# Kernel optimization log

Hardware: AMD Instinct MI355X
Metric: run time of the kernel (lower is better)

## Reference

```python
import jax, jax.numpy as jnp
import numpy as np

FEATURES = 1024
NUM_HEADS = 16
HEAD_SIZE = FEATURES // NUM_HEADS
B, T = 4, 2048
LN_EPS = 1e-6


def setup_inputs() -> dict:
    key = jax.random.key(0)
    ks = jax.random.split(key, 12)
    C, H, D = FEATURES, NUM_HEADS, HEAD_SIZE
    s_in = 1.0 / np.sqrt(C)
    s_ff = 1.0 / np.sqrt(4 * C)
    return {
        "x": jax.random.normal(ks[0], (B, T, C), jnp.float32),
        # per-head Q/K/V projections (no bias), stacked over heads
        "wq": jax.random.normal(ks[1], (H, C, D), jnp.float32) * s_in,
        "wk": jax.random.normal(ks[2], (H, C, D), jnp.float32) * s_in,
        "wv": jax.random.normal(ks[3], (H, C, D), jnp.float32) * s_in,
        "w_proj": jax.random.normal(ks[4], (C, C), jnp.float32) * s_in,
        "b_proj": jnp.zeros((C,), jnp.float32),
        "w_ff1": jax.random.normal(ks[5], (C, 4 * C), jnp.float32) * s_in,
        "b_ff1": jnp.zeros((4 * C,), jnp.float32),
        "w_ff2": jax.random.normal(ks[6], (4 * C, C), jnp.float32) * s_ff,
        "b_ff2": jnp.zeros((C,), jnp.float32),
        "ln1_scale": jnp.ones((C,), jnp.float32),
        "ln1_bias": jnp.zeros((C,), jnp.float32),
        "ln2_scale": jnp.ones((C,), jnp.float32),
        "ln2_bias": jnp.zeros((C,), jnp.float32),
    }


def _layernorm(x, scale, bias):
    mu = jnp.mean(x, axis=-1, keepdims=True)
    var = jnp.mean(jnp.square(x - mu), axis=-1, keepdims=True)
    return (x - mu) * jax.lax.rsqrt(var + LN_EPS) * scale + bias


def reference(x, wq, wk, wv, w_proj, b_proj, w_ff1, b_ff1, w_ff2, b_ff2,
              ln1_scale, ln1_bias, ln2_scale, ln2_bias):
    Bn, Tn, C = x.shape
    res = x
    xn = _layernorm(x, ln1_scale, ln1_bias)
    # per-head projections, vectorized over heads: [B,H,T,D]
    q = jnp.einsum('btc,hcd->bhtd', xn, wq)
    k = jnp.einsum('btc,hcd->bhtd', xn, wk)
    v = jnp.einsum('btc,hcd->bhtd', xn, wv)
    wei = jnp.einsum('bhtd,bhsd->bhts', q, k)
    tril = jnp.tril(jnp.ones((Tn, Tn), jnp.float32))
    # NOTE: original scales by C**-0.5 (full feature dim, not head_size),
    # and multiplies after masking (-inf * scale stays -inf).
    wei = jnp.where(tril == 0, -jnp.inf, wei) * (C ** -0.5)
    wei = jax.nn.softmax(wei, axis=-1)
    out = jnp.einsum('bhts,bhsd->bhtd', wei, v)
    # concat heads back to [B,T,C]
    out = out.transpose(0, 2, 1, 3).reshape(Bn, Tn, C)
    x = res + out @ w_proj + b_proj
    res = x
    xn = _layernorm(x, ln2_scale, ln2_bias)
    h = jax.nn.relu(xn @ w_ff1 + b_ff1)
    out = res + h @ w_ff2 + b_ff2
    return out
```

## Files before the change

kernel.cpp:

```cpp
#include <hip/hip_runtime.h>

#define Bn 4
#define Tn 2048
#define Cn 1024
#define Hn 16
#define Dn 64
#define Mr (Bn*Tn)

typedef _Float16 half8 __attribute__((ext_vector_type(8)));
typedef _Float16 half4v __attribute__((ext_vector_type(4)));
typedef float f32x4 __attribute__((ext_vector_type(4)));
typedef unsigned u32x4 __attribute__((ext_vector_type(4)));

__device__ __forceinline__ void g2l16(const void* g, void* l) {
  __builtin_amdgcn_global_load_lds((__attribute__((address_space(1))) void*)g,
                                   (__attribute__((address_space(3))) void*)l, 16, 0, 0);
}

#define SB  __builtin_amdgcn_sched_barrier(0)
#define BAR __builtin_amdgcn_s_barrier()
#define VMW8 asm volatile("s_waitcnt vmcnt(8)" ::: "memory")
#define VMW6 asm volatile("s_waitcnt vmcnt(6)" ::: "memory")
#define VMW4 asm volatile("s_waitcnt vmcnt(4)" ::: "memory")
#define VMW3 asm volatile("s_waitcnt vmcnt(3)" ::: "memory")
#define VMW0 asm volatile("s_waitcnt vmcnt(0)" ::: "memory")

__global__ __launch_bounds__(256) void transpose_f32_f16(const float* __restrict__ in,
                                                         _Float16* __restrict__ out,
                                                         int R, int C) {
  __shared__ float tile[32][33];
  const size_t zoff = (size_t)blockIdx.z * R * C;
  in += zoff; out += zoff;
  const int c0 = blockIdx.x * 32, r0 = blockIdx.y * 32;
  const int tx = threadIdx.x, ty = threadIdx.y;
#pragma unroll
  for (int i = 0; i < 4; ++i)
    tile[ty + i*8][tx] = in[(size_t)(r0 + ty + i*8) * C + c0 + tx];
  __syncthreads();
#pragma unroll
  for (int i = 0; i < 4; ++i)
    out[(size_t)(c0 + ty + i*8) * R + r0 + tx] = (_Float16)tile[tx][ty + i*8];
}

__global__ __launch_bounds__(256) void ln_row(const float* __restrict__ x,
                                              const float* __restrict__ g,
                                              const float* __restrict__ bta,
                                              _Float16* __restrict__ out) {
  const int row = blockIdx.x;
  const float4 v = ((const float4*)(x + (size_t)row * Cn))[threadIdx.x];
  float s  = v.x + v.y + v.z + v.w;
  float ss = v.x*v.x + v.y*v.y + v.z*v.z + v.w*v.w;
#pragma unroll
  for (int m = 1; m < 64; m <<= 1) { s += __shfl_xor(s, m); ss += __shfl_xor(ss, m); }
  __shared__ float red[8];
  const int wave = threadIdx.x >> 6, lane = threadIdx.x & 63;
  if (lane == 0) { red[wave] = s; red[4 + wave] = ss; }
  __syncthreads();
  s  = red[0] + red[1] + red[2] + red[3];
  ss = red[4] + red[5] + red[6] + red[7];
  const float mean = s * (1.0f/Cn);
  const float var  = ss * (1.0f/Cn) - mean*mean;
  const float rstd = rsqrtf(var + 1e-6f);
  const int c = threadIdx.x * 4;
  const float4 gg = ((const float4*)g)[threadIdx.x];
  const float4 bb = ((const float4*)bta)[threadIdx.x];
  half4v o;
  o[0] = (_Float16)((v.x - mean) * rstd * gg.x + bb.x);
  o[1] = (_Float16)((v.y - mean) * rstd * gg.y + bb.y);
  o[2] = (_Float16)((v.z - mean) * rstd * gg.z + bb.z);
  o[3] = (_Float16)((v.w - mean) * rstd * gg.w + bb.w);
  *((half4v*)(out + (size_t)row * Cn + c)) = o;
}

enum { EPI_QKV = 0, EPI_PROJ = 2, EPI_FF1 = 3, EPI_FF2 = 4 };

template<int BN, int EPI>
__global__ __launch_bounds__(512, 2) void gemm8p(const _Float16* __restrict__ A,
                                                 const _Float16* __restrict__ Bt,
                                                 void* __restrict__ outp,
                                                 void* __restrict__ out2,
                                                 void* __restrict__ out3,
                                                 const float* __restrict__ bias,
                                                 const float* __restrict__ resid,
                                                 int M, int N, int K, int nxg) {
  constexpr int NF = BN/64;
  constexpr int BSLOT = BN*32;
  __shared__ __align__(16) _Float16 Ar[4*256*32];
  __shared__ __align__(16) _Float16 Br[4*BSLOT];

  const int tid = threadIdx.x, wave = tid >> 6, lane = tid & 63;
  const int lr = lane & 15, lg = lane >> 4;
  const int sL = (lr & 3) ^ ((lr >> 2) & 3);
  const int laneoff = lr*32 + ((lg ^ sL) * 8);

  int lin = blockIdx.x;
  const int cpx = gridDim.x >> 3;
  lin = (lin & 7) * cpx + (lin >> 3);
  const int bx = lin % nxg, by = lin / nxg;
  const int brow = by * 256, bcol = bx * BN;
  const int wr = wave >> 2, wc = wave & 3;
  const int arow0 = wr * 128;
  const int bcol0 = wc * (BN/4);

  f32x4 acc[8][NF] = {};

  auto STAGE = [&](int st, int kh) {
    const int slot = (2*st + kh) & 3;
    const int koff = st*64 + kh*32;
#pragma unroll
    for (int i = 0; i < 2; ++i) {
      const int qc = i*512 + wave*64 + lane;
      const int row = qc >> 2;
      const int c = (qc & 3) ^ ((row & 3) ^ ((row >> 2) & 3));
      g2l16(A + (size_t)(brow + row)*K + koff + c*8,
            &Ar[slot*8192 + (i*512 + wave*64)*8]);
    }
#pragma unroll
    for (int i = 0; i < BN/128; ++i) {
      const int qc = i*512 + wave*64 + lane;
      const int row = qc >> 2;
      const int c = (qc & 3) ^ ((row & 3) ^ ((row >> 2) & 3));
      g2l16(Bt + (size_t)(bcol + row)*K + koff + c*8,
            &Br[slot*BSLOT + (i*512 + wave*64)*8]);
    }
  };
  auto RDA = [&](int slot, int mh, half8* af) {
#pragma unroll
    for (int i = 0; i < 4; ++i)
      af[i] = *(const half8*)(&Ar[slot*8192 + (arow0 + (mh*4 + i)*16)*32 + laneoff]);
  };
  auto RDB = [&](int slot, half8* bf) {
#pragma unroll
    for (int j = 0; j < NF; ++j)
      bf[j] = *(const half8*)(&Br[slot*BSLOT + (bcol0 + j*16)*32 + laneoff]);
  };

#define MMC(MH) do {                                                          \
    __builtin_amdgcn_s_setprio(1);                                            \
    _Pragma("unroll") for (int i_ = 0; i_ < 4; ++i_)                          \
      _Pragma("unroll") for (int j_ = 0; j_ < NF; ++j_)                       \
        acc[(MH)*4 + i_][j_] = __builtin_amdgcn_mfma_f32_16x16x32_f16(        \
            af[i_], bf[j_], acc[(MH)*4 + i_][j_], 0, 0, 0);                   \
    __builtin_amdgcn_s_setprio(0); } while (0)

  const int ns = K >> 6;
  STAGE(0, 0); STAGE(0, 1); STAGE(1, 0);
  if constexpr (BN == 256) VMW8; else VMW6;
  SB; BAR;

  half8 af[4], bf[NF];
  for (int s = 0; s < ns - 2; ++s) {
    const int s0 = (2*s) & 3, s1 = s0 + 1;
    RDB(s0, bf); RDA(s0, 0, af); STAGE(s + 1, 1);
    SB; BAR; MMC(0); SB; BAR;
    RDA(s0, 1, af);
    if constexpr (BN == 256) VMW8; else VMW6;
    SB; BAR; MMC(1); SB; BAR;
    RDB(s1, bf); RDA(s1, 0, af); STAGE(s + 2, 0);
    SB; BAR; MMC(0); SB; BAR;
    RDA(s1, 1, af);
    if constexpr (BN == 256) VMW8; else VMW6;
    SB; BAR; MMC(1); SB; BAR;
  }
  {
    const int s = ns - 2; const int s0 = (2*s) & 3, s1 = s0 + 1;
    RDB(s0, bf); RDA(s0, 0, af); STAGE(s + 1, 1);
    SB; BAR; MMC(0); SB; BAR;
    RDA(s0, 1, af);
    if constexpr (BN == 256) VMW8; else VMW6;
    SB; BAR; MMC(1); SB; BAR;
    RDB(s1, bf); RDA(s1, 0, af);
    SB; BAR; MMC(0); SB; BAR;
    RDA(s1, 1, af);
    if constexpr (BN == 256) VMW4; else VMW3;
    SB; BAR; MMC(1); SB; BAR;
  }
  {
    const int s = ns - 1; const int s0 = (2*s) & 3, s1 = s0 + 1;
    RDB(s0, bf); RDA(s0, 0, af);
    SB; BAR; MMC(0); SB; BAR;
    RDA(s0, 1, af);
    VMW0;
    SB; BAR; MMC(1); SB; BAR;
    RDB(s1, bf); RDA(s1, 0, af);
    SB; BAR; MMC(0); SB; BAR;
    RDA(s1, 1, af);
    SB; BAR; MMC(1); SB; BAR;
  }
#undef MMC

#pragma unroll
  for (int a = 0; a < 8; ++a) {
#pragma unroll
    for (int j = 0; j < NF; ++j) {
      const int col = bcol + bcol0 + j*16 + lr;
#pragma unroll
      for (int r = 0; r < 4; ++r) {
        const int row = brow + arow0 + a*16 + lg*4 + r;
        const float v = acc[a][j][r];
        if constexpr (EPI == EPI_QKV) {
          const int sel = col >> 10;
          const int cw = col & 1023;
          const int hh = cw >> 6, dd = cw & 63;
          const size_t bhh = (size_t)(row >> 11) * Hn + hh;
          const int t = row & 2047;
          if (sel == 0)      ((_Float16*)outp)[(bhh*Tn + t)*Dn + dd] = (_Float16)v;
          else if (sel == 1) ((_Float16*)out2)[(bhh*Tn + t)*Dn + dd] = (_Float16)v;
          else               ((_Float16*)out3)[(bhh*Dn + dd)*Tn + t] = (_Float16)v;
        } else if constexpr (EPI == EPI_PROJ || EPI == EPI_FF2) {
          ((float*)outp)[(size_t)row * N + col] = v + bias[col] + resid[(size_t)row * N + col];
        } else if constexpr (EPI == EPI_FF1) {
          const float t = v + bias[col];
          ((_Float16*)outp)[(size_t)row * N + col] = (_Float16)(t > 0.f ? t : 0.f);
        }
      }
    }
  }
}

__global__ __launch_bounds__(256) void attn_kernel(const _Float16* __restrict__ q,
                                                   const _Float16* __restrict__ k,
                                                   const _Float16* __restrict__ vt,
                                                   _Float16* __restrict__ out) {
  const int pi = blockIdx.x;
  const int qtA = pi * 128;
  const int qtB = (15 - pi) * 128;
  const int h = blockIdx.y, b = blockIdx.z;
  const int tid = threadIdx.x, wave = tid >> 6, lane = tid & 63;
  const int lr = lane & 15, lg = lane >> 4;
  const size_t bh = (size_t)b * Hn + h;
  const _Float16* qg = q  + bh * (Tn * Dn);
  const _Float16* kg = k  + bh * (Tn * Dn);
  const _Float16* vg = vt + bh * (Dn * Tn);

  __shared__ __align__(16) _Float16 Ks[2][64*64];
  __shared__ __align__(16) _Float16 Vs[2][64*64];

  const _Float16 qsc = (_Float16)0.03125f;
  half8 qfA[2][2], qfB[2][2];
#pragma unroll
  for (int qi = 0; qi < 2; ++qi)
#pragma unroll
    for (int dh = 0; dh < 2; ++dh) {
      half8 a = *(const half8*)(qg + (size_t)(qtA + wave*32 + qi*16 + lr)*Dn + dh*32 + lg*8);
      half8 c = *(const half8*)(qg + (size_t)(qtB + wave*32 + qi*16 + lr)*Dn + dh*32 + lg*8);
#pragma unroll
      for (int j = 0; j < 8; ++j) { a[j] *= qsc; c[j] *= qsc; }
      qfA[qi][dh] = a; qfB[qi][dh] = c;
    }

  f32x4 oaccA[2][4] = {}, oaccB[2][4] = {};
  float mrowA[2] = {-__builtin_inff(), -__builtin_inff()};
  float mrowB[2] = {-__builtin_inff(), -__builtin_inff()};
  float lsumA[2] = {0.f, 0.f}, lsumB[2] = {0.f, 0.f};

  const int ntB = (qtB >> 6) + 2;

  auto STAGE = [&](int bufi, int t) {
    const int kvt = t * 64;
#pragma unroll
    for (int r = 0; r < 2; ++r) {
      const int g0 = r*256 + wave*64;
      const int g  = g0 + lane;
      const int rr = g >> 3;
      const int cs = (g & 7) ^ (rr & 7);
      g2l16(kg + (size_t)(kvt + rr)*Dn + cs*8, &Ks[bufi][g0*8]);
      g2l16(vg + (size_t)rr*Tn + kvt + cs*8,   &Vs[bufi][g0*8]);
    }
  };

  auto COMPUTE = [&](const half8 (&qf)[2][2], f32x4 (&oacc)[2][4],
                     float* mrow, float* lsum, int qb,
                     const _Float16* KS, const _Float16* VS, int kvt) {
    half8 kb[4][2];
#pragma unroll
    for (int f = 0; f < 4; ++f)
#pragma unroll
      for (int dh = 0; dh < 2; ++dh)
        kb[f][dh] = *(const half8*)(KS + (16*f + lr)*64 + (((4*dh + lg) ^ (lr & 7)) * 8));

#pragma unroll
    for (int qi = 0; qi < 2; ++qi) {
      f32x4 sv[4];
#pragma unroll
      for (int f = 0; f < 4; ++f) {
        f32x4 tacc = {0.f, 0.f, 0.f, 0.f};
        tacc = __builtin_amdgcn_mfma_f32_16x16x32_f16(kb[f][0], qf[qi][0], tacc, 0, 0, 0);
        tacc = __builtin_amdgcn_mfma_f32_16x16x32_f16(kb[f][1], qf[qi][1], tacc, 0, 0, 0);
        sv[f] = tacc;
      }
      const int qrow = qb + wave*32 + qi*16 + lr;
#pragma unroll
      for (int f = 0; f < 4; ++f)
#pragma unroll
        for (int r = 0; r < 4; ++r) {
          const int kvv = kvt + 16*f + 4*lg + r;
          sv[f][r] = (kvv > qrow) ? -__builtin_inff() : sv[f][r];
        }
      float tm = sv[0][0];
#pragma unroll
      for (int f = 0; f < 4; ++f)
#pragma unroll
        for (int r = 0; r < 4; ++r) tm = fmaxf(tm, sv[f][r]);
      tm = fmaxf(tm, __shfl_xor(tm, 16));
      tm = fmaxf(tm, __shfl_xor(tm, 32));
      const float mn = fmaxf(mrow[qi], tm);
      const float alpha = __expf(mrow[qi] - mn);
      mrow[qi] = mn;
      float ps = 0.f;
#pragma unroll
      for (int f = 0; f < 4; ++f)
#pragma unroll
        for (int r = 0; r < 4; ++r) {
          const float e = __expf(sv[f][r] - mn);
          ps += e;
          sv[f][r] = e;
        }
      ps += __shfl_xor(ps, 16);
      ps += __shfl_xor(ps, 32);
      lsum[qi] = lsum[qi] * alpha + ps;
      unsigned ph[4][2];
#pragma unroll
      for (int f = 0; f < 4; ++f)
#pragma unroll
        for (int m = 0; m < 2; ++m) {
          const unsigned lo = (unsigned)__builtin_bit_cast(unsigned short, (_Float16)sv[f][2*m]);
          const unsigned hi = (unsigned)__builtin_bit_cast(unsigned short, (_Float16)sv[f][2*m + 1]);
          ph[f][m] = lo | (hi << 16);
        }
      float ab[4];
#pragma unroll
      for (int r = 0; r < 4; ++r) ab[r] = __shfl(alpha, 4*lg + r);
#pragma unroll
      for (int df = 0; df < 4; ++df)
#pragma unroll
        for (int r = 0; r < 4; ++r) oacc[qi][df][r] *= ab[r];
      const int s0 = lr + 16*(2*(lg & 1));
      const int s1 = s0 + 16;
      half8 pa[2];
#pragma unroll
      for (int kh = 0; kh < 2; ++kh) {
        u32x4 w = {0u, 0u, 0u, 0u};
#pragma unroll
        for (int fi = 0; fi < 2; ++fi) {
          const unsigned a0 = __shfl(ph[2*kh + fi][0], s0);
          const unsigned a1 = __shfl(ph[2*kh + fi][1], s0);
          const unsigned a2 = __shfl(ph[2*kh + fi][0], s1);
          const unsigned a3 = __shfl(ph[2*kh + fi][1], s1);
          const bool sel = ((lg >> 1) == fi);
          w[0] = sel ? a0 : w[0];
          w[1] = sel ? a1 : w[1];
          w[2] = sel ? a2 : w[2];
          w[3] = sel ? a3 : w[3];
        }
        pa[kh] = __builtin_bit_cast(half8, w);
      }
#pragma unroll
      for (int df = 0; df < 4; ++df) {
        half8 vb0 = *(const half8*)(VS + (16*df + lr)*64 + (((0 + lg) ^ (lr & 7)) * 8));
        half8 vb1 = *(const half8*)(VS + (16*df + lr)*64 + (((4 + lg) ^ (lr & 7)) * 8));
        oacc[qi][df] = __builtin_amdgcn_mfma_f32_16x16x32_f16(pa[0], vb0, oacc[qi][df], 0, 0, 0);
        oacc[qi][df] = __builtin_amdgcn_mfma_f32_16x16x32_f16(pa[1], vb1, oacc[qi][df], 0, 0, 0);
      }
    }
  };

  STAGE(0, 0);
  __syncthreads();

  for (int t = 0; t < ntB; ++t) {
    const int kvt = t * 64;
    if (t + 1 < ntB) STAGE((t + 1) & 1, t + 1);
    const _Float16* KS = Ks[t & 1];
    const _Float16* VS = Vs[t & 1];
    if (kvt <= qtA + wave*32 + 31) COMPUTE(qfA, oaccA, mrowA, lsumA, qtA, KS, VS, kvt);
    if (kvt <= qtB + wave*32 + 31) COMPUTE(qfB, oaccB, mrowB, lsumB, qtB, KS, VS, kvt);
    __syncthreads();
  }

  auto EPI = [&](const f32x4 (&oacc)[2][4], const float* lsum, int qb) {
#pragma unroll
    for (int qi = 0; qi < 2; ++qi) {
      const float linv = 1.0f / lsum[qi];
      float lb[4];
#pragma unroll
      for (int r = 0; r < 4; ++r) lb[r] = __shfl(linv, 4*lg + r);
#pragma unroll
      for (int df = 0; df < 4; ++df)
#pragma unroll
        for (int r = 0; r < 4; ++r) {
          const int row = qb + wave*32 + qi*16 + 4*lg + r;
          const int col = h*Dn + df*16 + lr;
          out[((size_t)b*Tn + row)*Cn + col] = (_Float16)(oacc[qi][df][r] * lb[r]);
        }
    }
  };
  EPI(oaccA, lsumA, qtA);
  EPI(oaccB, lsumB, qtB);
}

extern "C" void kernel_launch(void* const* d_in, const int* in_sizes, int n_in,
                              void* d_out, int out_size, void* d_ws, size_t ws_size,
                              hipStream_t stream) {
  const float* x      = (const float*)d_in[0];
  const float* wq     = (const float*)d_in[1];
  const float* wk     = (const float*)d_in[2];
  const float* wv     = (const float*)d_in[3];
  const float* w_proj = (const float*)d_in[4];
  const float* b_proj = (const float*)d_in[5];
  const float* w_ff1  = (const float*)d_in[6];
  const float* b_ff1  = (const float*)d_in[7];
  const float* w_ff2  = (const float*)d_in[8];
  const float* b_ff2  = (const float*)d_in[9];
  const float* ln1s   = (const float*)d_in[10];
  const float* ln1b   = (const float*)d_in[11];
  const float* ln2s   = (const float*)d_in[12];
  const float* ln2b   = (const float*)d_in[13];
  float* outp = (float*)d_out;

  char* ws = (char*)d_ws;
  constexpr size_t MB = (size_t)1 << 20;
  _Float16* Wq_t  = (_Float16*)(ws + 0*MB);
  _Float16* Wk_t  = (_Float16*)(ws + 2*MB);
  _Float16* Wv_t  = (_Float16*)(ws + 4*MB);
  _Float16* Wp_t  = (_Float16*)(ws + 6*MB);
  _Float16* Wf1_t = (_Float16*)(ws + 8*MB);
  _Float16* Wf2_t = (_Float16*)(ws + 16*MB);
  _Float16* xn    = (_Float16*)(ws + 24*MB);
  _Float16* attn_o= (_Float16*)(ws + 24*MB);
  _Float16* qbuf  = (_Float16*)(ws + 40*MB);
  _Float16* kbuf  = (_Float16*)(ws + 56*MB);
  _Float16* vtbuf = (_Float16*)(ws + 72*MB);
  _Float16* hbuf  = (_Float16*)(ws + 40*MB);
  float*    x2    = (float*)   (ws + 104*MB);
  _Float16* xn2   = (_Float16*)(ws + 136*MB);

  dim3 tb(32, 8);
  transpose_f32_f16<<<dim3(2, 32, 16), tb, 0, stream>>>(wq, Wq_t, 1024, 64);
  transpose_f32_f16<<<dim3(2, 32, 16), tb, 0, stream>>>(wk, Wk_t, 1024, 64);
  transpose_f32_f16<<<dim3(2, 32, 16), tb, 0, stream>>>(wv, Wv_t, 1024, 64);
  transpose_f32_f16<<<dim3(32, 32, 1), tb, 0, stream>>>(w_proj, Wp_t, 1024, 1024);
  transpose_f32_f16<<<dim3(128, 32, 1), tb, 0, stream>>>(w_ff1, Wf1_t, 1024, 4096);
  transpose_f32_f16<<<dim3(32, 128, 1), tb, 0, stream>>>(w_ff2, Wf2_t, 4096, 1024);

  ln_row<<<Mr, 256, 0, stream>>>(x, ln1s, ln1b, xn);

  gemm8p<256, EPI_QKV><<<dim3(384), 512, 0, stream>>>(xn, Wq_t, qbuf, kbuf, vtbuf,
                                                      nullptr, nullptr, Mr, 3*Cn, Cn, 12);

  attn_kernel<<<dim3(8, Hn, Bn), 256, 0, stream>>>(qbuf, kbuf, vtbuf, attn_o);

  gemm8p<128, EPI_PROJ><<<dim3(256), 512, 0, stream>>>(attn_o, Wp_t, x2, nullptr, nullptr,
                                                       b_proj, x, Mr, Cn, Cn, 8);

  ln_row<<<Mr, 256, 0, stream>>>(x2, ln2s, ln2b, xn2);

  gemm8p<256, EPI_FF1><<<dim3(512), 512, 0, stream>>>(xn2, Wf1_t, hbuf, nullptr, nullptr,
                                                      b_ff1, nullptr, Mr, 4*Cn, Cn, 16);
  gemm8p<128, EPI_FF2><<<dim3(256), 512, 0, stream>>>(hbuf, Wf2_t, outp, nullptr, nullptr,
                                                      b_ff2, x2, Mr, Cn, 4*Cn, 8);
}
```

Before: 592.7 us.

## Use exp2 softmax with lazy rescaling, skip masks off-diagonal, retile QKV GEMM

Folds log2(e) into the Q scale so softmax uses exp2f, and skips causal masking for tiles fully below the diagonal. It also rescales the output accumulators only when the running max grows beyond a threshold (lazy rescale), and packs probabilities with cvt_pkrtz. Separately it halves the QKV GEMM tile width to launch twice as many blocks. Lazy rescaling lets exponentials exceed 1 (up to about 2^11.5), which risks fp16 overflow or precision loss in P.

```diff
diff --git a/kernel.cpp b/kernel.cpp
--- a/kernel.cpp
+++ b/kernel.cpp
@@ -9,6 +9,7 @@
 
 typedef _Float16 half8 __attribute__((ext_vector_type(8)));
 typedef _Float16 half4v __attribute__((ext_vector_type(4)));
+typedef _Float16 half2v __attribute__((ext_vector_type(2)));
 typedef float f32x4 __attribute__((ext_vector_type(4)));
 typedef unsigned u32x4 __attribute__((ext_vector_type(4)));
 
@@ -236,7 +237,7 @@
   __shared__ __align__(16) _Float16 Ks[2][64*64];
   __shared__ __align__(16) _Float16 Vs[2][64*64];
 
-  const _Float16 qsc = (_Float16)0.03125f;
+  const _Float16 qsc = (_Float16)(0.03125f * 1.44269504f);
   half8 qfA[2][2], qfB[2][2];
 #pragma unroll
   for (int qi = 0; qi < 2; ++qi)
@@ -289,52 +290,53 @@
         tacc = __builtin_amdgcn_mfma_f32_16x16x32_f16(kb[f][1], qf[qi][1], tacc, 0, 0, 0);
         sv[f] = tacc;
       }
-      const int qrow = qb + wave*32 + qi*16 + lr;
-#pragma unroll
-      for (int f = 0; f < 4; ++f)
-#pragma unroll
-        for (int r = 0; r < 4; ++r) {
-          const int kvv = kvt + 16*f + 4*lg + r;
-          sv[f][r] = (kvv > qrow) ? -__builtin_inff() : sv[f][r];
-        }
-      float tm = sv[0][0];
-#pragma unroll
-      for (int f = 0; f < 4; ++f)
-#pragma unroll
-        for (int r = 0; r < 4; ++r) tm = fmaxf(tm, sv[f][r]);
+      const int rowbase = qb + wave*32 + qi*16;
+      const int qrow = rowbase + lr;
+      if (kvt + 63 > rowbase) {
+#pragma unroll
+        for (int f = 0; f < 4; ++f)
+#pragma unroll
+          for (int r = 0; r < 4; ++r) {
+            const int kvv = kvt + 16*f + 4*lg + r;
+            sv[f][r] = (kvv > qrow) ? -__builtin_inff() : sv[f][r];
+          }
+      }
+      float t0 = fmaxf(fmaxf(sv[0][0], sv[0][1]), fmaxf(sv[0][2], sv[0][3]));
+      float t1 = fmaxf(fmaxf(sv[1][0], sv[1][1]), fmaxf(sv[1][2], sv[1][3]));
+      float t2 = fmaxf(fmaxf(sv[2][0], sv[2][1]), fmaxf(sv[2][2], sv[2][3]));
+      float t3 = fmaxf(fmaxf(sv[3][0], sv[3][1]), fmaxf(sv[3][2], sv[3][3]));
+      float tm = fmaxf(fmaxf(t0, t1), fmaxf(t2, t3));
       tm = fmaxf(tm, __shfl_xor(tm, 16));
       tm = fmaxf(tm, __shfl_xor(tm, 32));
-      const float mn = fmaxf(mrow[qi], tm);
-      const float alpha = __expf(mrow[qi] - mn);
-      mrow[qi] = mn;
+      if (!__all(tm - mrow[qi] <= 11.5f)) {
+        const float mn = fmaxf(mrow[qi], tm);
+        const float alpha = exp2f(mrow[qi] - mn);
+        mrow[qi] = mn;
+        lsum[qi] *= alpha;
+        float ab[4];
+#pragma unroll
+        for (int r = 0; r < 4; ++r) ab[r] = __shfl(alpha, 4*lg + r);
+#pragma unroll
+        for (int df = 0; df < 4; ++df)
+#pragma unroll
+          for (int r = 0; r < 4; ++r) oacc[qi][df][r] *= ab[r];
+      }
+      const float mcur = mrow[qi];
       float ps = 0.f;
-#pragma unroll
-      for (int f = 0; f < 4; ++f)
-#pragma unroll
-        for (int r = 0; r < 4; ++r) {
-          const float e = __expf(sv[f][r] - mn);
-          ps += e;
-          sv[f][r] = e;
-        }
+      unsigned ph[4][2];
+#pragma unroll
+      for (int f = 0; f < 4; ++f) {
+        const float e0 = exp2f(sv[f][0] - mcur);
+        const float e1 = exp2f(sv[f][1] - mcur);
+        const float e2 = exp2f(sv[f][2] - mcur);
+        const float e3 = exp2f(sv[f][3] - mcur);
+        ps += (e0 + e1) + (e2 + e3);
+        ph[f][0] = __builtin_bit_cast(unsigned, __builtin_amdgcn_cvt_pkrtz(e0, e1));
+        ph[f][1] = __builtin_bit_cast(unsigned, __builtin_amdgcn_cvt_pkrtz(e2, e3));
+      }
       ps += __shfl_xor(ps, 16);
       ps += __shfl_xor(ps, 32);
-      lsum[qi] = lsum[qi] * alpha + ps;
-      unsigned ph[4][2];
-#pragma unroll
-      for (int f = 0; f < 4; ++f)
-#pragma unroll
-        for (int m = 0; m < 2; ++m) {
-          const unsigned lo = (unsigned)__builtin_bit_cast(unsigned short, (_Float16)sv[f][2*m]);
-          const unsigned hi = (unsigned)__builtin_bit_cast(unsigned short, (_Float16)sv[f][2*m + 1]);
-          ph[f][m] = lo | (hi << 16);
-        }
-      float ab[4];
-#pragma unroll
-      for (int r = 0; r < 4; ++r) ab[r] = __shfl(alpha, 4*lg + r);
-#pragma unroll
-      for (int df = 0; df < 4; ++df)
-#pragma unroll
-        for (int r = 0; r < 4; ++r) oacc[qi][df][r] *= ab[r];
+      lsum[qi] += ps;
       const int s0 = lr + 16*(2*(lg & 1));
       const int s1 = s0 + 16;
       half8 pa[2];
@@ -445,8 +447,8 @@
 
   ln_row<<<Mr, 256, 0, stream>>>(x, ln1s, ln1b, xn);
 
-  gemm8p<256, EPI_QKV><<<dim3(384), 512, 0, stream>>>(xn, Wq_t, qbuf, kbuf, vtbuf,
-                                                      nullptr, nullptr, Mr, 3*Cn, Cn, 12);
+  gemm8p<128, EPI_QKV><<<dim3(768), 512, 0, stream>>>(xn, Wq_t, qbuf, kbuf, vtbuf,
+                                                      nullptr, nullptr, Mr, 3*Cn, Cn, 24);
 
   attn_kernel<<<dim3(8, Hn, Bn), 256, 0, stream>>>(qbuf, kbuf, vtbuf, attn_o);
 
```

After: 616.8 us. 1.04x slower.
